# Kernel tuning notes

Hardware: AMD Instinct MI355X
Metric: run time of the kernel (lower is better)

Reference implementation:

```python
import jax, jax.numpy as jnp
import numpy as np
import math

B, S, H, NH, NKV, HD = 1, 2048, 4096, 32, 8, 128
ROPE_THETA = 10000.0


def setup_inputs() -> dict:
    key = jax.random.key(0)
    ks = jax.random.split(key, 16)
    hidden_states = jax.random.normal(ks[0], (B, S, H), jnp.float32) * 0.02
    Wq = jax.random.normal(ks[1], (NH * HD, H), jnp.float32) * 0.02
    Wk = jax.random.normal(ks[2], (NKV * HD, H), jnp.float32) * 0.02
    Wv = jax.random.normal(ks[3], (NKV * HD, H), jnp.float32) * 0.02
    Wo = jax.random.normal(ks[4], (H, NH * HD), jnp.float32) * 0.02
    # RoPE cos/sin, HF Llama convention: emb = concat(freqs, freqs)
    inv_freq = 1.0 / (ROPE_THETA ** (jnp.arange(0, HD, 2, dtype=jnp.float32) / HD))
    pos = jnp.arange(S, dtype=jnp.float32)
    freqs = pos[:, None] * inv_freq[None, :]              # [S, HD/2]
    emb = jnp.concatenate([freqs, freqs], axis=-1)        # [S, HD]
    cos = jnp.cos(emb)[None]                              # [1, S, HD]
    sin = jnp.sin(emb)[None]
    # additive causal mask [B, 1, S, S]
    causal = jnp.tril(jnp.ones((S, S), dtype=bool))
    attention_mask = jnp.where(causal, 0.0, -1e9).astype(jnp.float32)[None, None]
    # reorder permutations (as written by GPTQ act-order reordering)
    perm = lambda k, n: jax.random.permutation(k, n).astype(jnp.int32)
    return {
        'hidden_states': hidden_states, 'Wq': Wq, 'Wk': Wk, 'Wv': Wv, 'Wo': Wo,
        'cos': cos, 'sin': sin, 'attention_mask': attention_mask,
        'q_order_col': perm(ks[5], H), 'q_order_row': perm(ks[6], NH * HD),
        'k_order_col': perm(ks[7], H), 'k_order_row': perm(ks[8], NKV * HD),
        'v_order_col': perm(ks[9], H), 'v_order_row': perm(ks[10], NKV * HD),
        'o_order_col': perm(ks[11], NH * HD), 'o_order_row': perm(ks[12], H),
    }


def _rotate_half(x):
    x1, x2 = jnp.split(x, 2, axis=-1)
    return jnp.concatenate([-x2, x1], axis=-1)


def reference(hidden_states, Wq, Wk, Wv, Wo, cos, sin, attention_mask,
              q_order_col, q_order_row, k_order_col, k_order_row,
              v_order_col, v_order_row, o_order_col, o_order_row):
    bsz, q_len, _ = hidden_states.shape
    # permuted projections: gather cols of input, GEMM, gather rows of output
    q = hidden_states[:, :, q_order_col] @ Wq.T
    q = q[:, :, q_order_row]
    k = hidden_states[:, :, k_order_col] @ Wk.T
    k = k[:, :, k_order_row]
    v = hidden_states[:, :, v_order_col] @ Wv.T
    v = v[:, :, v_order_row]
    q = q.reshape(bsz, q_len, NH, HD).transpose(0, 2, 1, 3)   # [B,NH,S,HD]
    k = k.reshape(bsz, q_len, NKV, HD).transpose(0, 2, 1, 3)  # [B,NKV,S,HD]
    v = v.reshape(bsz, q_len, NKV, HD).transpose(0, 2, 1, 3)
    # RoPE
    c = cos[:, None, :, :]  # [1,1,S,HD]
    s = sin[:, None, :, :]
    q = q * c + _rotate_half(q) * s
    k = k * c + _rotate_half(k) * s
    # repeat_kv for GQA
    rep = NH // NKV
    k = jnp.repeat(k, rep, axis=1)  # [B,NH,S,HD]
    v = jnp.repeat(v, rep, axis=1)
    # eager attention: full score matrix, fp32 softmax
    scores = jnp.einsum('bhqd,bhkd->bhqk', q, k) / math.sqrt(HD)
    scores = scores + attention_mask
    probs = jax.nn.softmax(scores.astype(jnp.float32), axis=-1).astype(q.dtype)
    # dropout p=0.0 (eval) -> identity
    attn = jnp.einsum('bhqk,bhkd->bhqd', probs, v)
    attn = attn.transpose(0, 2, 1, 3).reshape(bsz, q_len, NH * HD)
    out = attn[:, :, o_order_col] @ Wo.T
    out = out[:, :, o_order_row]
    return out
```

## Files before the change

### kernel.cpp

```cpp
#include <hip/hip_runtime.h>

typedef unsigned short u16;
typedef unsigned char u8;
typedef __bf16 bf16x8 __attribute__((ext_vector_type(8)));
typedef float f32x4 __attribute__((ext_vector_type(4)));
typedef int i32x4 __attribute__((ext_vector_type(4)));
typedef int i32x8 __attribute__((ext_vector_type(8)));

__device__ __forceinline__ u16 f2bf(float f) {
    unsigned u = __float_as_uint(f);
    unsigned r = (u + 0x7fffu + ((u >> 16) & 1u)) >> 16;
    return (u16)r;
}
__device__ __forceinline__ float bf2f(u16 h) {
    return __uint_as_float(((unsigned)h) << 16);
}
__device__ __forceinline__ unsigned pack_bf2(float lo, float hi) {
    unsigned a = __float_as_uint(hi) + 0x8000u;
    unsigned b = __float_as_uint(lo) + 0x8000u;
    return __builtin_amdgcn_perm(a, b, 0x07060302u);
}
__device__ __forceinline__ unsigned pack_fp8x4(float a, float b, float c, float d) {
    unsigned w = __builtin_amdgcn_cvt_pk_fp8_f32(a, b, 0, false);
    w = __builtin_amdgcn_cvt_pk_fp8_f32(c, d, w, true);
    return w;
}
__device__ __forceinline__ void async_copy16(const void* g, void* l) {
    __builtin_amdgcn_global_load_lds((__attribute__((address_space(1))) void*)(void*)g,
                                     (__attribute__((address_space(3))) void*)l, 16, 0, 0);
}

#define FP8_SCALE 64.0f
#define FP8_UNSCALE (1.0f / 4096.0f)


__global__ void inv4_k(const int* __restrict__ q, const int* __restrict__ k,
                       const int* __restrict__ v, const int* __restrict__ o,
                       int* __restrict__ invq, int* __restrict__ invk,
                       int* __restrict__ invv, int* __restrict__ invo) {
    int i = blockIdx.x * 256 + threadIdx.x;
    int a = i >> 12, j = i & 4095;
    const int* p = a == 0 ? q : a == 1 ? k : a == 2 ? v : o;
    int* inv = a == 0 ? invq : a == 1 ? invk : a == 2 ? invv : invo;
    inv[p[j]] = j;
}

__global__ __launch_bounds__(256) void permw4_k(
    const float* __restrict__ Wq, const float* __restrict__ Wk,
    const float* __restrict__ Wv, const float* __restrict__ Wo,
    const int* __restrict__ qor, const int* __restrict__ kor,
    const int* __restrict__ vor, const int* __restrict__ oor,
    const int* __restrict__ invq, const int* __restrict__ invk,
    const int* __restrict__ invv, const int* __restrict__ invo,
    u8* __restrict__ Wqkf8, u16* __restrict__ Wvp, u16* __restrict__ Wop) {
    __shared__ float rowbuf[4096];
    int j = blockIdx.x;
    const float* W; const int* rp; const int* inv; int row; int f8;
    u8* out8 = nullptr; u16* out16 = nullptr;
    if (j < 4096)      { W = Wq; rp = qor; inv = invq; row = j;        out8 = Wqkf8 + (size_t)j * 4096; f8 = 1; }
    else if (j < 5120) { W = Wk; rp = kor; inv = invk; row = j - 4096; out8 = Wqkf8 + (size_t)j * 4096; f8 = 1; }
    else if (j < 6144) { W = Wv; rp = vor; inv = invv; row = j - 5120; out16 = Wvp + (size_t)(j - 5120) * 4096; f8 = 0; }
    else               { W = Wo; rp = oor; inv = invo; row = j - 6144; out16 = Wop + (size_t)(j - 6144) * 4096; f8 = 0; }
    if (f8) {
        int hd = row & 127, b = hd >> 4;
        row = (row & ~127) | ((hd & 15) | ((b & 1) << 6) | ((b & 2) << 3) | ((hd & 64) >> 1));
    }
    const float4* wr4 = (const float4*)(W + (size_t)rp[row] * 4096);
#pragma unroll
    for (int t = 0; t < 4; t++)
        ((float4*)rowbuf)[threadIdx.x + t * 256] = wr4[threadIdx.x + t * 256];
    __syncthreads();
    if (f8) {
        int t = threadIdx.x;
        const int4* inv4p = (const int4*)inv;
        float v[16];
#pragma unroll
        for (int u = 0; u < 4; u++) {
            int4 ix = inv4p[t * 4 + u];
            v[4 * u + 0] = rowbuf[ix.x] * FP8_SCALE;
            v[4 * u + 1] = rowbuf[ix.y] * FP8_SCALE;
            v[4 * u + 2] = rowbuf[ix.z] * FP8_SCALE;
            v[4 * u + 3] = rowbuf[ix.w] * FP8_SCALE;
        }
        uint4 wv;
        wv.x = pack_fp8x4(v[0], v[1], v[2], v[3]);
        wv.y = pack_fp8x4(v[4], v[5], v[6], v[7]);
        wv.z = pack_fp8x4(v[8], v[9], v[10], v[11]);
        wv.w = pack_fp8x4(v[12], v[13], v[14], v[15]);
        int tb = (t & ~7) | ((t & 7) ^ (j & 7));
        ((uint4*)out8)[tb] = wv;
    } else {
        unsigned* o32 = (unsigned*)out16;
        const int2* inv2 = (const int2*)inv;
#pragma unroll
        for (int t = 0; t < 8; t++) {
            int c = threadIdx.x + t * 256;
            int2 ij = inv2[c];
            o32[c] = pack_bf2(rowbuf[ij.x], rowbuf[ij.y]);
        }
    }
}

__global__ __launch_bounds__(256) void cvt_k(const float* __restrict__ x,
                                             u16* __restrict__ Xb,
                                             u8* __restrict__ Xf8) {
    int row = blockIdx.x;
    int t = threadIdx.x;
    const float4* src = (const float4*)(x + (size_t)row * 4096);
    float v[16];
#pragma unroll
    for (int u = 0; u < 4; u++) {
        float4 a = src[t * 4 + u];
        v[4 * u + 0] = a.x; v[4 * u + 1] = a.y; v[4 * u + 2] = a.z; v[4 * u + 3] = a.w;
    }
    uint4 b0, b1;
    b0.x = pack_bf2(v[0], v[1]);  b0.y = pack_bf2(v[2], v[3]);
    b0.z = pack_bf2(v[4], v[5]);  b0.w = pack_bf2(v[6], v[7]);
    b1.x = pack_bf2(v[8], v[9]);  b1.y = pack_bf2(v[10], v[11]);
    b1.z = pack_bf2(v[12], v[13]); b1.w = pack_bf2(v[14], v[15]);
    uint4* ob = (uint4*)(Xb + (size_t)row * 4096);
    ob[t * 2] = b0;
    ob[t * 2 + 1] = b1;
    uint4 w8;
    w8.x = pack_fp8x4(v[0] * FP8_SCALE, v[1] * FP8_SCALE, v[2] * FP8_SCALE, v[3] * FP8_SCALE);
    w8.y = pack_fp8x4(v[4] * FP8_SCALE, v[5] * FP8_SCALE, v[6] * FP8_SCALE, v[7] * FP8_SCALE);
    w8.z = pack_fp8x4(v[8] * FP8_SCALE, v[9] * FP8_SCALE, v[10] * FP8_SCALE, v[11] * FP8_SCALE);
    w8.w = pack_fp8x4(v[12] * FP8_SCALE, v[13] * FP8_SCALE, v[14] * FP8_SCALE, v[15] * FP8_SCALE);
    int tb = (t & ~7) | ((t & 7) ^ (row & 7));
    ((uint4*)(Xf8 + (size_t)row * 4096))[tb] = w8;
}

__global__ __launch_bounds__(256) void vtr_k(const float* __restrict__ Vpart,
                                             u16* __restrict__ Vt) {
    __shared__ u16 t[64][65];
    int bx = blockIdx.x;
    int s0 = (bx & 31) * 64, c0 = (bx >> 5) * 64;
    int x = threadIdx.x & 63, y4 = threadIdx.x >> 6;
    const float* Vp0 = Vpart;
    const float* Vp1 = Vpart + (size_t)2048 * 1024;
    for (int i = 0; i < 16; i++) {
        int r = y4 * 16 + i;
        size_t idx = (size_t)(s0 + r) * 1024 + c0 + x;
        t[r][x] = f2bf(Vp0[idx] + Vp1[idx]);
    }
    __syncthreads();
    for (int i = 0; i < 16; i++) {
        int r = y4 * 16 + i;
        int xk = 4 * (x & 15) + (x >> 4);
        Vt[(size_t)(c0 + r) * 2048 + s0 + xk] = t[x][r];
    }
}


__global__ __launch_bounds__(256) void gemm_qkv_k(const u8* __restrict__ Xf8,
                                                  const u16* __restrict__ Xb,
                                                  const u8* __restrict__ Wqk,
                                                  const u16* __restrict__ Wv,
                                                  u16* __restrict__ QKV,
                                                  float* __restrict__ Vpart,
                                                  const float* __restrict__ cosv,
                                                  const float* __restrict__ sinv) {
    __shared__ u8 lds[32768];
    const int tid = threadIdx.x;
    const int w = tid >> 6, lane = tid & 63;
    const int quad = lane >> 4, l16 = lane & 15;
    const int bm0 = blockIdx.y * 128;
    const int wm = (w >> 1) * 64, wn = (w & 1) * 64;
    if (blockIdx.x < 40) {
        const int bn0 = blockIdx.x * 128;
        u8* ldsA = lds;
        u8* ldsB = lds + 16384;
        const u8* Ag = Xf8 + (size_t)(bm0 + w * 32 + (lane >> 3)) * 4096 + (lane & 7) * 16;
        const u8* Bg = Wqk + (size_t)(bn0 + w * 32 + (lane >> 3)) * 4096 + (lane & 7) * 16;
        u8* la = ldsA + w * 32 * 128;
        u8* lb = ldsB + w * 32 * 128;
        const int swz = l16 & 7;
        f32x4 acc[4][4] = {};
        for (int k0 = 0; k0 < 4096; k0 += 128) {
#pragma unroll
            for (int t = 0; t < 4; t++) async_copy16(Ag + (size_t)t * 8 * 4096 + k0, la + t * 1024);
#pragma unroll
            for (int t = 0; t < 4; t++) async_copy16(Bg + (size_t)t * 8 * 4096 + k0, lb + t * 1024);
            __syncthreads();
            i32x8 af[4], bf[4];
#pragma unroll
            for (int i = 0; i < 4; i++) {
                int r = wm + i * 16 + l16;
                union { i32x8 v8; i32x4 v4[2]; } u;
                u.v4[0] = *(const i32x4*)&ldsA[r * 128 + ((quad * 2) ^ swz) * 16];
                u.v4[1] = *(const i32x4*)&ldsA[r * 128 + ((quad * 2 + 1) ^ swz) * 16];
                af[i] = u.v8;
            }
#pragma unroll
            for (int j = 0; j < 4; j++) {
                int r = wn + j * 16 + l16;
                union { i32x8 v8; i32x4 v4[2]; } u;
                u.v4[0] = *(const i32x4*)&ldsB[r * 128 + ((quad * 2) ^ swz) * 16];
                u.v4[1] = *(const i32x4*)&ldsB[r * 128 + ((quad * 2 + 1) ^ swz) * 16];
                bf[j] = u.v8;
            }
#pragma unroll
            for (int i = 0; i < 4; i++)
#pragma unroll
                for (int j = 0; j < 4; j++)
                    acc[i][j] = __builtin_amdgcn_mfma_scale_f32_16x16x128_f8f6f4(
                        af[i], bf[j], acc[i][j], 0, 0,
                        0, 0x7F7F7F7F, 0, 0x7F7F7F7F);
            __syncthreads();
        }
        const float qsc = (bn0 < 4096) ? 0.08838834764831845f : 1.0f;
        const int hb = (wn ? 32 : 0) + l16;
#pragma unroll
        for (int i = 0; i < 4; i++) {
            const int row = bm0 + wm + i * 16 + quad * 4;
#pragma unroll
            for (int jp = 0; jp < 2; jp++) {
                const int d1 = hb + jp * 16;
                const int ce = bn0 + wn + jp * 32 + l16;
#pragma unroll
                for (int r = 0; r < 4; r++) {
                    const int s = row + r;
                    const float c  = cosv[s * 128 + d1];
                    const float sn = sinv[s * 128 + d1];
                    const float x1 = acc[i][jp * 2][r]     * FP8_UNSCALE;
                    const float x2 = acc[i][jp * 2 + 1][r] * FP8_UNSCALE;
                    QKV[(size_t)s * 6144 + ce]      = f2bf((x1 * c - x2 * sn) * qsc);
                    QKV[(size_t)s * 6144 + ce + 16] = f2bf((x2 * c + x1 * sn) * qsc);
                }
            }
        }
    } else {
        const int vx = blockIdx.x - 40;
        const int bn0 = (vx & 7) * 128;
        const int kslice = vx >> 3;
        const int kb = kslice * 2048;
        u16* lds_a0 = (u16*)lds;
        u16* lds_a1 = (u16*)(lds + 8192);
        u16* lds_b0 = (u16*)(lds + 16384);
        u16* lds_b1 = (u16*)(lds + 24576);
        const int r0 = w * 16 + (lane >> 2);
        const int c0 = (lane & 3) * 8;
        const u16* Ag = Xb + (size_t)(bm0 + r0) * 4096 + kb + c0;
        const u16* Bg = Wv + (size_t)(bn0 + r0) * 4096 + kb + c0;
        f32x4 acc[4][4] = {};
        for (int k0 = 0; k0 < 2048; k0 += 64) {
            async_copy16(Ag + k0,                         lds_a0 + w * 512);
            async_copy16(Ag + (size_t)64 * 4096 + k0,     lds_a0 + (w + 4) * 512);
            async_copy16(Ag + k0 + 32,                    lds_a1 + w * 512);
            async_copy16(Ag + (size_t)64 * 4096 + k0 + 32, lds_a1 + (w + 4) * 512);
            async_copy16(Bg + k0,                         lds_b0 + w * 512);
            async_copy16(Bg + (size_t)64 * 4096 + k0,     lds_b0 + (w + 4) * 512);
            async_copy16(Bg + k0 + 32,                    lds_b1 + w * 512);
            async_copy16(Bg + (size_t)64 * 4096 + k0 + 32, lds_b1 + (w + 4) * 512);
            __syncthreads();
#pragma unroll
            for (int kk = 0; kk < 2; kk++) {
                const u16* la = kk ? lds_a1 : lds_a0;
                const u16* lb = kk ? lds_b1 : lds_b0;
                bf16x8 af[4], bfv[4];
#pragma unroll
                for (int i = 0; i < 4; i++)
                    af[i] = *(const bf16x8*)&la[(wm + i * 16 + l16) * 32 + quad * 8];
#pragma unroll
                for (int j = 0; j < 4; j++)
                    bfv[j] = *(const bf16x8*)&lb[(wn + j * 16 + l16) * 32 + quad * 8];
#pragma unroll
                for (int i = 0; i < 4; i++)
#pragma unroll
                    for (int j = 0; j < 4; j++)
                        acc[i][j] = __builtin_amdgcn_mfma_f32_16x16x32_bf16(af[i], bfv[j], acc[i][j], 0, 0, 0);
            }
            __syncthreads();
        }
        float* Vp = Vpart + (size_t)kslice * 2048 * 1024;
#pragma unroll
        for (int i = 0; i < 4; i++) {
            const int row = bm0 + wm + i * 16 + quad * 4;
#pragma unroll
            for (int j = 0; j < 4; j++) {
                const int col = bn0 + wn + j * 16 + l16;
#pragma unroll
                for (int r = 0; r < 4; r++)
                    Vp[(size_t)(row + r) * 1024 + col] = acc[i][j][r];
            }
        }
    }
}


#define GO_STAGE(bufi, kt) do {                                                   \
    u16* la_ = S + (bufi) * 24576;                                                \
    u16* lb_ = la_ + 16384;                                                       \
    const int k0_ = (kt) * 64;                                                    \
    _Pragma("unroll")                                                             \
    for (int u = 0; u < 4; u++)                                                   \
        async_copy16(Asrc + (size_t)u * 64 * 4096 + k0_, la_ + u * 4096 + sdst);  \
    _Pragma("unroll")                                                             \
    for (int u = 0; u < 2; u++)                                                   \
        async_copy16(Bsrc + (size_t)u * 64 * 4096 + k0_, lb_ + u * 4096 + sdst);  \
} while (0)

#define GO_COMPUTE(bufi) do {                                                     \
    const u16* la_ = S + (bufi) * 24576;                                          \
    const u16* lb_ = la_ + 16384;                                                 \
    bf16x8 bfr[4][2], afr[2][2];                                                  \
    _Pragma("unroll")                                                             \
    for (int j = 0; j < 4; j++) {                                                 \
        const int rb_ = (wn + j * 16 + l16) * 64;                                 \
        bfr[j][0] = *(const bf16x8*)&lb_[rb_ + o0];                               \
        bfr[j][1] = *(const bf16x8*)&lb_[rb_ + o1];                               \
    }                                                                             \
    _Pragma("unroll")                                                             \
    for (int i = 0; i < 2; i++) {                                                 \
        const int ra_ = (wm + i * 16 + l16) * 64;                                 \
        afr[i][0] = *(const bf16x8*)&la_[ra_ + o0];                               \
        afr[i][1] = *(const bf16x8*)&la_[ra_ + o1];                               \
    }                                                                             \
    asm volatile("s_waitcnt lgkmcnt(0)" ::: "memory");                            \
    __builtin_amdgcn_sched_barrier(0);                                            \
    __builtin_amdgcn_s_setprio(1);                                                \
    _Pragma("unroll")                                                             \
    for (int i = 0; i < 2; i++)                                                   \
        _Pragma("unroll")                                                         \
        for (int j = 0; j < 4; j++) {                                             \
            acc[i][j] = __builtin_amdgcn_mfma_f32_16x16x32_bf16(afr[i][0], bfr[j][0], acc[i][j], 0, 0, 0); \
            acc[i][j] = __builtin_amdgcn_mfma_f32_16x16x32_bf16(afr[i][1], bfr[j][1], acc[i][j], 0, 0, 0); \
        }                                                                         \
    __builtin_amdgcn_s_setprio(0);                                                \
    _Pragma("unroll")                                                             \
    for (int i = 0; i < 2; i++) {                                                 \
        const int ra_ = (wm + (i + 2) * 16 + l16) * 64;                           \
        afr[i][0] = *(const bf16x8*)&la_[ra_ + o0];                               \
        afr[i][1] = *(const bf16x8*)&la_[ra_ + o1];                               \
    }                                                                             \
    asm volatile("s_waitcnt lgkmcnt(0)" ::: "memory");                            \
    __builtin_amdgcn_sched_barrier(0);                                            \
    __builtin_amdgcn_s_setprio(1);                                                \
    _Pragma("unroll")                                                             \
    for (int i = 0; i < 2; i++)                                                   \
        _Pragma("unroll")                                                         \
        for (int j = 0; j < 4; j++) {                                             \
            acc[i + 2][j] = __builtin_amdgcn_mfma_f32_16x16x32_bf16(afr[i][0], bfr[j][0], acc[i + 2][j], 0, 0, 0); \
            acc[i + 2][j] = __builtin_amdgcn_mfma_f32_16x16x32_bf16(afr[i][1], bfr[j][1], acc[i + 2][j], 0, 0, 0); \
        }                                                                         \
    __builtin_amdgcn_s_setprio(0);                                                \
} while (0)

#define GO_BAR() asm volatile("s_barrier" ::: "memory")

__global__ __launch_bounds__(512, 2) void gemm_o_k(const u16* __restrict__ A,
                                                   const u16* __restrict__ B,
                                                   float* __restrict__ Out) {
    extern __shared__ u16 S[];
    const int tid = threadIdx.x;
    const int w = tid >> 6, lane = tid & 63;
    const int quad = lane >> 4, l16 = lane & 15;
    const int linear = blockIdx.y * 32 + blockIdx.x;
    const int wgid = (linear & 7) * 32 + (linear >> 3);
    const int bm0 = (wgid >> 5) * 256;
    const int bn0 = (wgid & 31) * 128;
    const int wm = (w >> 1) * 64;
    const int wn = (w & 1) * 64;
    const int sr = tid >> 3;
    const int scg = ((tid & 7) ^ (sr & 7)) * 8;
    const int sdst = tid * 8;
    const u16* Asrc = A + (size_t)(bm0 + sr) * 4096 + scg;
    const u16* Bsrc = B + (size_t)(bn0 + sr) * 4096 + scg;
    const int swz = l16 & 7;
    const int o0 = (quad ^ swz) * 8;
    const int o1 = ((4 | quad) ^ swz) * 8;

    f32x4 acc[4][4] = {};

    GO_STAGE(0, 0);
    GO_STAGE(1, 1);
    GO_STAGE(2, 2);
    asm volatile("s_waitcnt vmcnt(12)" ::: "memory");
    GO_BAR();

    int cur = 0;
    for (int t = 0; t < 61; ++t) {
        GO_COMPUTE(cur);
        GO_BAR();
        GO_STAGE(cur, t + 3);
        asm volatile("s_waitcnt vmcnt(12)" ::: "memory");
        GO_BAR();
        cur = (cur == 2) ? 0 : cur + 1;
    }
    GO_COMPUTE(1);
    asm volatile("s_waitcnt vmcnt(6)" ::: "memory");
    GO_BAR();
    GO_COMPUTE(2);
    asm volatile("s_waitcnt vmcnt(0)" ::: "memory");
    GO_BAR();
    GO_COMPUTE(0);

#pragma unroll
    for (int i = 0; i < 4; i++) {
        const int row = bm0 + wm + i * 16 + quad * 4;
#pragma unroll
        for (int j = 0; j < 4; j++) {
            const int col = bn0 + wn + j * 16 + l16;
#pragma unroll
            for (int r = 0; r < 4; r++)
                Out[(size_t)(row + r) * 4096 + col] = acc[i][j][r];
        }
    }
}


__global__ __launch_bounds__(256) void attn_k(const u16* __restrict__ Qb,
                                              const u16* __restrict__ Kb,
                                              const u16* __restrict__ Vt,
                                              u16* __restrict__ Ob,
                                              int qstride, int kstride) {
    __shared__ u16 ldsK[4 * 64 * 32];
    __shared__ u16 ldsV[2 * 128 * 32];
    __shared__ u16 ldsP[4][32 * 72];
    const int h = blockIdx.x;
    const int qt = (int)gridDim.y - 1 - (int)blockIdx.y;
    const int kvh = h >> 2;
    const int tid = threadIdx.x;
    const int w = tid >> 6, lane = tid & 63;
    const int quad = lane >> 4, l16 = lane & 15;
    const int q0 = qt * 128;
    const int wrow = q0 + w * 32;

    bf16x8 qf[2][4];
#pragma unroll
    for (int mi = 0; mi < 2; mi++)
#pragma unroll
        for (int kk = 0; kk < 4; kk++)
            qf[mi][kk] = *(const bf16x8*)&Qb[(size_t)(wrow + mi * 16 + l16) * qstride +
                                             h * 128 + kk * 32 + quad * 8];

    const u16* kp[4]; const u16* vp[4];
    u16* ldk[4]; u16* ldv[4];
#pragma unroll
    for (int t = 0; t < 4; t++) {
        int wl = w + t * 4;
        int kk = wl >> 2, part = wl & 3;
        kp[t] = Kb + (size_t)(part * 16 + (lane >> 2)) * kstride + kvh * 128 + kk * 32 + (lane & 3) * 8;
        int ks2 = wl >> 3, p2 = wl & 7;
        vp[t] = Vt + (size_t)(kvh * 128 + p2 * 16 + (lane >> 2)) * 2048 + ks2 * 32 + (lane & 3) * 8;
        ldk[t] = ldsK + wl * 512;
        ldv[t] = ldsV + wl * 512;
    }

    f32x4 acc_o[2][8] = {};
    float lrow[2][4] = {};

    const int nk = 2 * (qt + 1);
    for (int kn = 0; kn < nk; kn++) {
        const int g0 = kn * 64;
#pragma unroll
        for (int t = 0; t < 4; t++) async_copy16(kp[t], ldk[t]);
#pragma unroll
        for (int t = 0; t < 4; t++) async_copy16(vp[t], ldv[t]);
#pragma unroll
        for (int t = 0; t < 4; t++) { kp[t] += (size_t)64 * kstride; vp[t] += 64; }
        __syncthreads();

        if (g0 <= wrow + 31) {
            f32x4 accs[2][4] = {};
#pragma unroll
            for (int kk = 0; kk < 4; kk++) {
                bf16x8 bfrag[4];
#pragma unroll
                for (int ni = 0; ni < 4; ni++)
                    bfrag[ni] = *(const bf16x8*)&ldsK[kk * 2048 + (ni * 16 + l16) * 32 + quad * 8];
#pragma unroll
                for (int mi = 0; mi < 2; mi++)
#pragma unroll
                    for (int ni = 0; ni < 4; ni++)
                        accs[mi][ni] = __builtin_amdgcn_mfma_f32_16x16x32_bf16(
                            qf[mi][kk], bfrag[ni], accs[mi][ni], 0, 0, 0);
            }
            const bool diag = (g0 + 63 > wrow);
            int kidx[4];
#pragma unroll
            for (int ni = 0; ni < 4; ni++) kidx[ni] = g0 + ni * 16 + l16;
#pragma unroll
            for (int mi = 0; mi < 2; mi++) {
#pragma unroll
                for (int r = 0; r < 4; r++) {
                    const int qrow = wrow + mi * 16 + quad * 4 + r;
                    float p[4];
#pragma unroll
                    for (int ni = 0; ni < 4; ni++) {
                        float s = accs[mi][ni][r];
                        if (diag && (kidx[ni] > qrow)) s = -1e30f;
                        p[ni] = __expf(s);
                    }
                    lrow[mi][r] += (p[0] + p[1]) + (p[2] + p[3]);
                    uint2 pk;
                    pk.x = pack_bf2(p[0], p[1]);
                    pk.y = pack_bf2(p[2], p[3]);
                    *(uint2*)&ldsP[w][(mi * 16 + quad * 4 + r) * 72 + l16 * 4] = pk;
                }
            }
#pragma unroll
            for (int ks = 0; ks < 2; ks++) {
                bf16x8 pa[2];
#pragma unroll
                for (int mi = 0; mi < 2; mi++)
                    pa[mi] = *(const bf16x8*)&ldsP[w][(mi * 16 + l16) * 72 + ks * 32 + quad * 8];
#pragma unroll
                for (int oj = 0; oj < 8; oj++) {
                    bf16x8 vb = *(const bf16x8*)&ldsV[ks * 4096 + (oj * 16 + l16) * 32 + quad * 8];
#pragma unroll
                    for (int mi = 0; mi < 2; mi++)
                        acc_o[mi][oj] = __builtin_amdgcn_mfma_f32_16x16x32_bf16(
                            pa[mi], vb, acc_o[mi][oj], 0, 0, 0);
                }
            }
        }
        __syncthreads();
    }
#pragma unroll
    for (int mi = 0; mi < 2; mi++)
#pragma unroll
        for (int r = 0; r < 4; r++) {
            float l = lrow[mi][r];
            l += __shfl_xor(l, 1);
            l += __shfl_xor(l, 2);
            l += __shfl_xor(l, 4);
            l += __shfl_xor(l, 8);
            const float inv = 1.0f / l;
            const int qrow = wrow + mi * 16 + quad * 4 + r;
#pragma unroll
            for (int oj = 0; oj < 8; oj++)
                Ob[(size_t)qrow * 4096 + h * 128 + oj * 16 + l16] =
                    f2bf(acc_o[mi][oj][r] * inv);
        }
}


extern "C" void kernel_launch(void* const* d_in, const int* in_sizes, int n_in,
                              void* d_out, int out_size, void* d_ws, size_t ws_size,
                              hipStream_t stream) {
    (void)in_sizes; (void)n_in; (void)out_size; (void)ws_size;
    const float* hidden = (const float*)d_in[0];
    const float* Wq = (const float*)d_in[1];
    const float* Wk = (const float*)d_in[2];
    const float* Wv = (const float*)d_in[3];
    const float* Wo = (const float*)d_in[4];
    const float* cosv = (const float*)d_in[5];
    const float* sinv = (const float*)d_in[6];
    const int* qoc = (const int*)d_in[8];
    const int* qor = (const int*)d_in[9];
    const int* koc = (const int*)d_in[10];
    const int* kor = (const int*)d_in[11];
    const int* voc = (const int*)d_in[12];
    const int* vor = (const int*)d_in[13];
    const int* ooc = (const int*)d_in[14];
    const int* oor = (const int*)d_in[15];

    char* ws = (char*)d_ws;
    size_t off = 0;
    int* invq = (int*)(ws + off); off += 16384;
    int* invk = (int*)(ws + off); off += 16384;
    int* invv = (int*)(ws + off); off += 16384;
    int* invo = (int*)(ws + off); off += 16384;
    u16* Wop   = (u16*)(ws + off); off += (size_t)4096 * 4096 * 2;
    u16* Xb    = (u16*)(ws + off); off += (size_t)2048 * 4096 * 2;
    u8*  Wqkf8 = (u8*)(ws + off);  off += (size_t)5120 * 4096;
    u16* Wvp   = (u16*)(ws + off); off += (size_t)1024 * 4096 * 2;
    u8*  Xf8   = (u8*)(ws + off);  off += (size_t)2048 * 4096;
    u16* QKVb  = (u16*)(ws + off); off += (size_t)2048 * 6144 * 2;
    u16* Vtb   = (u16*)(ws + off); off += (size_t)1024 * 2048 * 2;
    float* Vpart = (float*)(ws + off); off += (size_t)2 * 2048 * 1024 * 4;
    u16* Attb  = Xb;

    inv4_k<<<64, 256, 0, stream>>>(qoc, koc, voc, ooc, invq, invk, invv, invo);
    permw4_k<<<10240, 256, 0, stream>>>(Wq, Wk, Wv, Wo, qor, kor, vor, oor,
                                        invq, invk, invv, invo, Wqkf8, Wvp, Wop);
    cvt_k<<<2048, 256, 0, stream>>>(hidden, Xb, Xf8);

    gemm_qkv_k<<<dim3(56, 16), 256, 0, stream>>>(Xf8, Xb, Wqkf8, Wvp, QKVb, Vpart,
                                                 cosv, sinv);

    vtr_k<<<512, 256, 0, stream>>>(Vpart, Vtb);

    attn_k<<<dim3(32, 16), 256, 0, stream>>>(QKVb, QKVb + 4096, Vtb, Attb, 6144, 6144);

    gemm_o_k<<<dim3(32, 8), 512, 147456, stream>>>(Attb, Wop, (float*)d_out);
}
```

Baseline: 485.3 us.

## Triple-buffer QKV GEMM with 512-thread blocks and explicit waitcnt pipelining

```diff
diff --git a/kernel.cpp b/kernel.cpp
--- a/kernel.cpp
+++ b/kernel.cpp
@@ -152,81 +152,156 @@
 }
 
 
-__global__ __launch_bounds__(256) void gemm_qkv_k(const u8* __restrict__ Xf8,
-                                                  const u16* __restrict__ Xb,
-                                                  const u8* __restrict__ Wqk,
-                                                  const u16* __restrict__ Wv,
-                                                  u16* __restrict__ QKV,
-                                                  float* __restrict__ Vpart,
-                                                  const float* __restrict__ cosv,
-                                                  const float* __restrict__ sinv) {
-    __shared__ u8 lds[32768];
+#define QKV_BAR() asm volatile("s_barrier" ::: "memory")
+
+#define QK_STAGE(bufi, kt) do {                                                   \
+    u8* d_ = S8 + (bufi) * 32768 + tid * 16;                                      \
+    const int k0_ = (kt) * 128;                                                   \
+    async_copy16(AgQ + k0_, d_);                                                  \
+    async_copy16(AgQ + (size_t)64 * 4096 + k0_, d_ + 8192);                       \
+    async_copy16(BgQ + k0_, d_ + 16384);                                          \
+    async_copy16(BgQ + (size_t)64 * 4096 + k0_, d_ + 24576);                      \
+} while (0)
+
+#define QK_COMPUTE(bufi) do {                                                     \
+    const u8* la_ = S8 + (bufi) * 32768;                                          \
+    const u8* lb_ = la_ + 16384;                                                  \
+    i32x8 af0, af1, bf0, bf1;                                                     \
+    union { i32x8 v8; i32x4 v4[2]; } u_;                                          \
+    int R_ = (wn + l16) * 128;                                                    \
+    u_.v4[0] = *(const i32x4*)&lb_[R_ + s0b];                                     \
+    u_.v4[1] = *(const i32x4*)&lb_[R_ + s1b]; bf0 = u_.v8;                        \
+    R_ = (wn + 16 + l16) * 128;                                                   \
+    u_.v4[0] = *(const i32x4*)&lb_[R_ + s0b];                                     \
+    u_.v4[1] = *(const i32x4*)&lb_[R_ + s1b]; bf1 = u_.v8;                        \
+    R_ = (wm + l16) * 128;                                                        \
+    u_.v4[0] = *(const i32x4*)&la_[R_ + s0b];                                     \
+    u_.v4[1] = *(const i32x4*)&la_[R_ + s1b]; af0 = u_.v8;                        \
+    R_ = (wm + 16 + l16) * 128;                                                   \
+    u_.v4[0] = *(const i32x4*)&la_[R_ + s0b];                                     \
+    u_.v4[1] = *(const i32x4*)&la_[R_ + s1b]; af1 = u_.v8;                        \
+    asm volatile("s_waitcnt lgkmcnt(0)" ::: "memory");                            \
+    __builtin_amdgcn_sched_barrier(0);                                            \
+    __builtin_amdgcn_s_setprio(1);                                                \
+    acc[0][0] = __builtin_amdgcn_mfma_scale_f32_16x16x128_f8f6f4(af0, bf0, acc[0][0], 0, 0, 0, 0x7F7F7F7F, 0, 0x7F7F7F7F); \
+    acc[0][1] = __builtin_amdgcn_mfma_scale_f32_16x16x128_f8f6f4(af0, bf1, acc[0][1], 0, 0, 0, 0x7F7F7F7F, 0, 0x7F7F7F7F); \
+    acc[1][0] = __builtin_amdgcn_mfma_scale_f32_16x16x128_f8f6f4(af1, bf0, acc[1][0], 0, 0, 0, 0x7F7F7F7F, 0, 0x7F7F7F7F); \
+    acc[1][1] = __builtin_amdgcn_mfma_scale_f32_16x16x128_f8f6f4(af1, bf1, acc[1][1], 0, 0, 0, 0x7F7F7F7F, 0, 0x7F7F7F7F); \
+    __builtin_amdgcn_s_setprio(0);                                                \
+    R_ = (wm + 32 + l16) * 128;                                                   \
+    u_.v4[0] = *(const i32x4*)&la_[R_ + s0b];                                     \
+    u_.v4[1] = *(const i32x4*)&la_[R_ + s1b]; af0 = u_.v8;                        \
+    R_ = (wm + 48 + l16) * 128;                                                   \
+    u_.v4[0] = *(const i32x4*)&la_[R_ + s0b];                                     \
+    u_.v4[1] = *(const i32x4*)&la_[R_ + s1b]; af1 = u_.v8;                        \
+    asm volatile("s_waitcnt lgkmcnt(0)" ::: "memory");                            \
+    __builtin_amdgcn_sched_barrier(0);                                            \
+    __builtin_amdgcn_s_setprio(1);                                                \
+    acc[2][0] = __builtin_amdgcn_mfma_scale_f32_16x16x128_f8f6f4(af0, bf0, acc[2][0], 0, 0, 0, 0x7F7F7F7F, 0, 0x7F7F7F7F); \
+    acc[2][1] = __builtin_amdgcn_mfma_scale_f32_16x16x128_f8f6f4(af0, bf1, acc[2][1], 0, 0, 0, 0x7F7F7F7F, 0, 0x7F7F7F7F); \
+    acc[3][0] = __builtin_amdgcn_mfma_scale_f32_16x16x128_f8f6f4(af1, bf0, acc[3][0], 0, 0, 0, 0x7F7F7F7F, 0, 0x7F7F7F7F); \
+    acc[3][1] = __builtin_amdgcn_mfma_scale_f32_16x16x128_f8f6f4(af1, bf1, acc[3][1], 0, 0, 0, 0x7F7F7F7F, 0, 0x7F7F7F7F); \
+    __builtin_amdgcn_s_setprio(0);                                                \
+} while (0)
+
+#define V_STAGE(bufi, kt) do {                                                    \
+    u8* d_ = S8 + (bufi) * 32768 + tid * 16;                                      \
+    const int k0_ = (kt) * 64;                                                    \
+    async_copy16(AgV + k0_, d_);                                                  \
+    async_copy16(AgV + (size_t)64 * 4096 + k0_, d_ + 8192);                       \
+    async_copy16(BgV + k0_, d_ + 16384);                                          \
+    async_copy16(BgV + (size_t)64 * 4096 + k0_, d_ + 24576);                      \
+} while (0)
+
+#define V_COMPUTE(bufi) do {                                                      \
+    const u16* la_ = (const u16*)(S8 + (bufi) * 32768);                           \
+    const u16* lb_ = la_ + 8192;                                                  \
+    _Pragma("unroll")                                                             \
+    for (int kk_ = 0; kk_ < 2; kk_++) {                                           \
+        const int so_ = ((kk_ * 4 + quad) ^ swz) * 8;                             \
+        bf16x8 bv0 = *(const bf16x8*)&lb_[(wn + l16) * 64 + so_];                 \
+        bf16x8 bv1 = *(const bf16x8*)&lb_[(wn + 16 + l16) * 64 + so_];            \
+        bf16x8 a0 = *(const bf16x8*)&la_[(wm + l16) * 64 + so_];                  \
+        bf16x8 a1 = *(const bf16x8*)&la_[(wm + 16 + l16) * 64 + so_];             \
+        bf16x8 a2 = *(const bf16x8*)&la_[(wm + 32 + l16) * 64 + so_];             \
+        bf16x8 a3 = *(const bf16x8*)&la_[(wm + 48 + l16) * 64 + so_];             \
+        asm volatile("s_waitcnt lgkmcnt(0)" ::: "memory");                        \
+        __builtin_amdgcn_sched_barrier(0);                                        \
+        __builtin_amdgcn_s_setprio(1);                                            \
+        acc[0][0] = __builtin_amdgcn_mfma_f32_16x16x32_bf16(a0, bv0, acc[0][0], 0, 0, 0); \
+        acc[0][1] = __builtin_amdgcn_mfma_f32_16x16x32_bf16(a0, bv1, acc[0][1], 0, 0, 0); \
+        acc[1][0] = __builtin_amdgcn_mfma_f32_16x16x32_bf16(a1, bv0, acc[1][0], 0, 0, 0); \
+        acc[1][1] = __builtin_amdgcn_mfma_f32_16x16x32_bf16(a1, bv1, acc[1][1], 0, 0, 0); \
+        acc[2][0] = __builtin_amdgcn_mfma_f32_16x16x32_bf16(a2, bv0, acc[2][0], 0, 0, 0); \
+        acc[2][1] = __builtin_amdgcn_mfma_f32_16x16x32_bf16(a2, bv1, acc[2][1], 0, 0, 0); \
+        acc[3][0] = __builtin_amdgcn_mfma_f32_16x16x32_bf16(a3, bv0, acc[3][0], 0, 0, 0); \
+        acc[3][1] = __builtin_amdgcn_mfma_f32_16x16x32_bf16(a3, bv1, acc[3][1], 0, 0, 0); \
+        __builtin_amdgcn_s_setprio(0);                                            \
+    }                                                                             \
+} while (0)
+
+__global__ __launch_bounds__(512, 2) void gemm_qkv_k(const u8* __restrict__ Xf8,
+                                                     const u16* __restrict__ Xb,
+                                                     const u8* __restrict__ Wqk,
+                                                     const u16* __restrict__ Wv,
+                                                     u16* __restrict__ QKV,
+                                                     float* __restrict__ Vpart,
+                                                     const float* __restrict__ cosv,
+                                                     const float* __restrict__ sinv) {
+    extern __shared__ u8 S8[];
     const int tid = threadIdx.x;
     const int w = tid >> 6, lane = tid & 63;
     const int quad = lane >> 4, l16 = lane & 15;
     const int bm0 = blockIdx.y * 128;
-    const int wm = (w >> 1) * 64, wn = (w & 1) * 64;
+    const int wm = (w >> 2) * 64;
+    const int wn = (w & 3) * 32;
+    const int swz = l16 & 7;
+    const int s0b = ((quad * 2) ^ swz) * 16;
+    const int s1b = ((quad * 2 + 1) ^ swz) * 16;
+
     if (blockIdx.x < 40) {
         const int bn0 = blockIdx.x * 128;
-        u8* ldsA = lds;
-        u8* ldsB = lds + 16384;
-        const u8* Ag = Xf8 + (size_t)(bm0 + w * 32 + (lane >> 3)) * 4096 + (lane & 7) * 16;
-        const u8* Bg = Wqk + (size_t)(bn0 + w * 32 + (lane >> 3)) * 4096 + (lane & 7) * 16;
-        u8* la = ldsA + w * 32 * 128;
-        u8* lb = ldsB + w * 32 * 128;
-        const int swz = l16 & 7;
-        f32x4 acc[4][4] = {};
-        for (int k0 = 0; k0 < 4096; k0 += 128) {
-#pragma unroll
-            for (int t = 0; t < 4; t++) async_copy16(Ag + (size_t)t * 8 * 4096 + k0, la + t * 1024);
-#pragma unroll
-            for (int t = 0; t < 4; t++) async_copy16(Bg + (size_t)t * 8 * 4096 + k0, lb + t * 1024);
-            __syncthreads();
-            i32x8 af[4], bf[4];
-#pragma unroll
-            for (int i = 0; i < 4; i++) {
-                int r = wm + i * 16 + l16;
-                union { i32x8 v8; i32x4 v4[2]; } u;
-                u.v4[0] = *(const i32x4*)&ldsA[r * 128 + ((quad * 2) ^ swz) * 16];
-                u.v4[1] = *(const i32x4*)&ldsA[r * 128 + ((quad * 2 + 1) ^ swz) * 16];
-                af[i] = u.v8;
-            }
-#pragma unroll
-            for (int j = 0; j < 4; j++) {
-                int r = wn + j * 16 + l16;
-                union { i32x8 v8; i32x4 v4[2]; } u;
-                u.v4[0] = *(const i32x4*)&ldsB[r * 128 + ((quad * 2) ^ swz) * 16];
-                u.v4[1] = *(const i32x4*)&ldsB[r * 128 + ((quad * 2 + 1) ^ swz) * 16];
-                bf[j] = u.v8;
-            }
-#pragma unroll
-            for (int i = 0; i < 4; i++)
-#pragma unroll
-                for (int j = 0; j < 4; j++)
-                    acc[i][j] = __builtin_amdgcn_mfma_scale_f32_16x16x128_f8f6f4(
-                        af[i], bf[j], acc[i][j], 0, 0,
-                        0, 0x7F7F7F7F, 0, 0x7F7F7F7F);
-            __syncthreads();
-        }
+        const u8* AgQ = Xf8 + (size_t)(bm0 + (tid >> 3)) * 4096 + (tid & 7) * 16;
+        const u8* BgQ = Wqk + (size_t)(bn0 + (tid >> 3)) * 4096 + (tid & 7) * 16;
+        f32x4 acc[4][2] = {};
+
+        QK_STAGE(0, 0);
+        QK_STAGE(1, 1);
+        QK_STAGE(2, 2);
+        asm volatile("s_waitcnt vmcnt(8)" ::: "memory");
+        QKV_BAR();
+        int cur = 0;
+        for (int t = 0; t < 29; ++t) {
+            QK_COMPUTE(cur);
+            QKV_BAR();
+            QK_STAGE(cur, t + 3);
+            asm volatile("s_waitcnt vmcnt(8)" ::: "memory");
+            QKV_BAR();
+            cur = (cur == 2) ? 0 : cur + 1;
+        }
+        QK_COMPUTE(2);
+        asm volatile("s_waitcnt vmcnt(4)" ::: "memory");
+        QKV_BAR();
+        QK_COMPUTE(0);
+        asm volatile("s_waitcnt vmcnt(0)" ::: "memory");
+        QKV_BAR();
+        QK_COMPUTE(1);
+
         const float qsc = (bn0 < 4096) ? 0.08838834764831845f : 1.0f;
-        const int hb = (wn ? 32 : 0) + l16;
+        const int d1 = (w & 3) * 16 + l16;
+        const int col0 = bn0 + wn + l16;
 #pragma unroll
         for (int i = 0; i < 4; i++) {
             const int row = bm0 + wm + i * 16 + quad * 4;
 #pragma unroll
-            for (int jp = 0; jp < 2; jp++) {
-                const int d1 = hb + jp * 16;
-                const int ce = bn0 + wn + jp * 32 + l16;
-#pragma unroll
-                for (int r = 0; r < 4; r++) {
-                    const int s = row + r;
-                    const float c  = cosv[s * 128 + d1];
-                    const float sn = sinv[s * 128 + d1];
-                    const float x1 = acc[i][jp * 2][r]     * FP8_UNSCALE;
-                    const float x2 = acc[i][jp * 2 + 1][r] * FP8_UNSCALE;
-                    QKV[(size_t)s * 6144 + ce]      = f2bf((x1 * c - x2 * sn) * qsc);
-                    QKV[(size_t)s * 6144 + ce + 16] = f2bf((x2 * c + x1 * sn) * qsc);
-                }
+            for (int r = 0; r < 4; r++) {
+                const int s = row + r;
+                const float c  = cosv[s * 128 + d1];
+                const float sn = sinv[s * 128 + d1];
+                const float x1 = acc[i][0][r] * FP8_UNSCALE;
+                const float x2 = acc[i][1][r] * FP8_UNSCALE;
+                QKV[(size_t)s * 6144 + col0]      = f2bf((x1 * c - x2 * sn) * qsc);
+                QKV[(size_t)s * 6144 + col0 + 16] = f2bf((x2 * c + x1 * sn) * qsc);
             }
         }
     } else {
@@ -234,50 +309,40 @@
         const int bn0 = (vx & 7) * 128;
         const int kslice = vx >> 3;
         const int kb = kslice * 2048;
-        u16* lds_a0 = (u16*)lds;
-        u16* lds_a1 = (u16*)(lds + 8192);
-        u16* lds_b0 = (u16*)(lds + 16384);
-        u16* lds_b1 = (u16*)(lds + 24576);
-        const int r0 = w * 16 + (lane >> 2);
-        const int c0 = (lane & 3) * 8;
-        const u16* Ag = Xb + (size_t)(bm0 + r0) * 4096 + kb + c0;
-        const u16* Bg = Wv + (size_t)(bn0 + r0) * 4096 + kb + c0;
-        f32x4 acc[4][4] = {};
-        for (int k0 = 0; k0 < 2048; k0 += 64) {
-            async_copy16(Ag + k0,                         lds_a0 + w * 512);
-            async_copy16(Ag + (size_t)64 * 4096 + k0,     lds_a0 + (w + 4) * 512);
-            async_copy16(Ag + k0 + 32,                    lds_a1 + w * 512);
-            async_copy16(Ag + (size_t)64 * 4096 + k0 + 32, lds_a1 + (w + 4) * 512);
-            async_copy16(Bg + k0,                         lds_b0 + w * 512);
-            async_copy16(Bg + (size_t)64 * 4096 + k0,     lds_b0 + (w + 4) * 512);
-            async_copy16(Bg + k0 + 32,                    lds_b1 + w * 512);
-            async_copy16(Bg + (size_t)64 * 4096 + k0 + 32, lds_b1 + (w + 4) * 512);
-            __syncthreads();
-#pragma unroll
-            for (int kk = 0; kk < 2; kk++) {
-                const u16* la = kk ? lds_a1 : lds_a0;
-                const u16* lb = kk ? lds_b1 : lds_b0;
-                bf16x8 af[4], bfv[4];
-#pragma unroll
-                for (int i = 0; i < 4; i++)
-                    af[i] = *(const bf16x8*)&la[(wm + i * 16 + l16) * 32 + quad * 8];
-#pragma unroll
-                for (int j = 0; j < 4; j++)
-                    bfv[j] = *(const bf16x8*)&lb[(wn + j * 16 + l16) * 32 + quad * 8];
-#pragma unroll
-                for (int i = 0; i < 4; i++)
-#pragma unroll
-                    for (int j = 0; j < 4; j++)
-                        acc[i][j] = __builtin_amdgcn_mfma_f32_16x16x32_bf16(af[i], bfv[j], acc[i][j], 0, 0, 0);
-            }
-            __syncthreads();
-        }
+        const int srow = tid >> 3;
+        const int sblk = (tid & 7) ^ (srow & 7);
+        const u16* AgV = Xb + (size_t)(bm0 + srow) * 4096 + kb + sblk * 8;
+        const u16* BgV = Wv + (size_t)(bn0 + srow) * 4096 + kb + sblk * 8;
+        f32x4 acc[4][2] = {};
+
+        V_STAGE(0, 0);
+        V_STAGE(1, 1);
+        V_STAGE(2, 2);
+        asm volatile("s_waitcnt vmcnt(8)" ::: "memory");
+        QKV_BAR();
+        int cur = 0;
+        for (int t = 0; t < 29; ++t) {
+            V_COMPUTE(cur);
+            QKV_BAR();
+            V_STAGE(cur, t + 3);
+            asm volatile("s_waitcnt vmcnt(8)" ::: "memory");
+            QKV_BAR();
+            cur = (cur == 2) ? 0 : cur + 1;
+        }
+        V_COMPUTE(2);
+        asm volatile("s_waitcnt vmcnt(4)" ::: "memory");
+        QKV_BAR();
+        V_COMPUTE(0);
+        asm volatile("s_waitcnt vmcnt(0)" ::: "memory");
+        QKV_BAR();
+        V_COMPUTE(1);
+
         float* Vp = Vpart + (size_t)kslice * 2048 * 1024;
 #pragma unroll
         for (int i = 0; i < 4; i++) {
             const int row = bm0 + wm + i * 16 + quad * 4;
 #pragma unroll
-            for (int j = 0; j < 4; j++) {
+            for (int j = 0; j < 2; j++) {
                 const int col = bn0 + wn + j * 16 + l16;
 #pragma unroll
                 for (int r = 0; r < 4; r++)
@@ -577,8 +642,8 @@
                                         invq, invk, invv, invo, Wqkf8, Wvp, Wop);
     cvt_k<<<2048, 256, 0, stream>>>(hidden, Xb, Xf8);
 
-    gemm_qkv_k<<<dim3(56, 16), 256, 0, stream>>>(Xf8, Xb, Wqkf8, Wvp, QKVb, Vpart,
-                                                 cosv, sinv);
+    gemm_qkv_k<<<dim3(56, 16), 512, 98304, stream>>>(Xf8, Xb, Wqkf8, Wvp, QKVb, Vpart,
+                                                     cosv, sinv);
 
     vtr_k<<<512, 256, 0, stream>>>(Vpart, Vtb);
 
```

Result: slower. 498.0 us (+2.6%).
